# Performance work log

Measured on AMD Instinct MI355X. Metric: run time of the kernel, lower is better.

The kernel has to match this reference:

```python
import jax, jax.numpy as jnp
import numpy as np

B, L, C, K, NLEV, VOCAB, OUT = 32, 1024, 512, 2, 4, 128, 11


def setup_inputs() -> dict:
    key = jax.random.key(0)
    ks = jax.random.split(key, 8)
    x = jax.random.randint(ks[0], (B, L), 0, VOCAB, dtype=jnp.int32)
    mask = jax.random.randint(ks[1], (B, L), 0, 2).astype(jnp.bool_)
    emb = jax.random.uniform(ks[2], (VOCAB, C), minval=-0.5, maxval=0.5, dtype=jnp.float32)
    w1 = jax.random.normal(ks[3], (NLEV, C, C, K), dtype=jnp.float32) * 0.02
    b1 = jnp.zeros((NLEV, C), dtype=jnp.float32)
    w2 = jax.random.normal(ks[4], (NLEV, C, C, K), dtype=jnp.float32) * 0.02
    b2 = jnp.zeros((NLEV, C), dtype=jnp.float32)
    dec_w = jax.random.uniform(ks[5], (OUT, C), minval=-0.5, maxval=0.5, dtype=jnp.float32)
    dec_b = jnp.zeros((OUT,), dtype=jnp.float32)
    return dict(x=x, mask=mask, emb=emb, w1=w1, b1=b1, w2=w2, b2=b2, dec_w=dec_w, dec_b=dec_b)


def _causal_conv(h, w, b, dilation):
    # h: [B, C, L], w: [Cout, Cin, K]; left-pad (K-1)*d == conv+chomp in TCN
    pad = (w.shape[-1] - 1) * dilation
    out = jax.lax.conv_general_dilated(
        h, w, window_strides=(1,), padding=[(pad, 0)],
        rhs_dilation=(dilation,), dimension_numbers=("NCH", "OIH", "NCH"))
    return out + b[None, :, None]


def reference(x, mask, emb, w1, b1, w2, b2, dec_w, dec_b):
    h = emb[x].transpose(0, 2, 1)  # [B, C, L]
    for i in range(NLEV):  # fixed small number of TCN levels
        d = 2 ** i
        res = h
        h = jax.nn.relu(_causal_conv(h, w1[i], b1[i], d))
        h = jax.nn.relu(_causal_conv(h, w2[i], b2[i], d))
        h = jax.nn.relu(h + res)  # residual (in==out channels -> identity shortcut)
    y = jnp.einsum("bcl,oc->blo", h, dec_w) + dec_b  # [B, L, OUT]
    # mask-gather: original keeps only mask-true positions; zero others (jit-safe)
    return y * mask[..., None].astype(y.dtype)
```

## Files before the change

### kernel.cpp

```cpp
#include <hip/hip_runtime.h>
#include <stdint.h>

#define BB 32
#define LL 1024
#define CC 512
#define NN (BB * LL)
#define NLEVS 4
#define OUTD 11
#define LPAD 8
#define LROWS (LL + LPAD)

typedef __attribute__((ext_vector_type(8))) short bf16x8;
typedef __attribute__((ext_vector_type(4))) float f32x4;

static __device__ __forceinline__ unsigned short f2bf(float f) {
    union { float f; uint32_t u; } v; v.f = f;
    uint32_t u = v.u;
    uint32_t r = (u + 0x7fffu + ((u >> 16) & 1u)) >> 16;
    return (unsigned short)r;
}
static __device__ __forceinline__ float bf2f(unsigned short h) {
    union { uint32_t u; float f; } v; v.u = ((uint32_t)h) << 16;
    return v.f;
}

static __device__ __forceinline__ void llds16(const unsigned short* g, unsigned short* l) {
    __builtin_amdgcn_global_load_lds(
        (const __attribute__((address_space(1))) unsigned int*)g,
        (__attribute__((address_space(3))) unsigned int*)l, 16, 0, 0);
}

__global__ __launch_bounds__(256) void zero_pad_kernel(
    unsigned short* __restrict__ Hb0, unsigned short* __restrict__ Hb1)
{
    int t = blockIdx.x * 256 + threadIdx.x;
    unsigned short* base = (t >> 14) ? Hb1 : Hb0;
    int rem = t & 16383;
    int p = rem >> 9;
    int q = rem & 511;
    size_t off = (size_t)p * (LROWS * CC) + (size_t)q * 8;
    *(uint4*)(base + off) = (uint4){0u, 0u, 0u, 0u};
}

__global__ __launch_bounds__(256) void embed_kernel(
    const int* __restrict__ x, const float* __restrict__ emb,
    unsigned short* __restrict__ Hb0)
{
    int t = blockIdx.x * 256 + threadIdx.x;
    int n = t >> 6;
    int c8 = (t & 63) * 8;
    int idx = x[n];
    const float* src = emb + (size_t)idx * CC + c8;
    float4 v0 = *(const float4*)src;
    float4 v1 = *(const float4*)(src + 4);
    ushort4 a, b;
    a.x = f2bf(v0.x); a.y = f2bf(v0.y); a.z = f2bf(v0.z); a.w = f2bf(v0.w);
    b.x = f2bf(v1.x); b.y = f2bf(v1.y); b.z = f2bf(v1.z); b.w = f2bf(v1.w);
    int prow = (n >> 10) * LROWS + LPAD + (n & (LL - 1));
    unsigned short* dst = Hb0 + (size_t)prow * CC + c8;
    *(ushort4*)dst = a;
    *(ushort4*)(dst + 4) = b;
}

__global__ __launch_bounds__(256) void pack_w_kernel(
    const float* __restrict__ w1, const float* __restrict__ w2, unsigned short* __restrict__ WpT)
{
    int e = blockIdx.x * 256 + threadIdx.x;
    int cv = e >> 19;
    int r = e & 524287;
    int j = r >> 12;
    int co = (r >> 3) & 511;
    int h = r & 7;
    int kidx = j * 8 + h;
    int k = (kidx < 512) ? 1 : 0;
    int ci = kidx & 511;
    int lvl = cv >> 1;
    const float* w = (cv & 1) ? w2 : w1;
    float val = w[(((size_t)(lvl * 512 + co) * 512) + ci) * 2 + k];
    WpT[e] = f2bf(val);
}

template <bool HAS_RES>
__global__ __launch_bounds__(256, 4) void conv_gemm(
    const unsigned short* __restrict__ Ain, const unsigned short* __restrict__ WpT,
    const float* __restrict__ bias, const unsigned short* __restrict__ resB,
    unsigned short* __restrict__ OutB, int d)
{
    __shared__ unsigned short sA[136 * 64];

    const int tid = threadIdx.x;
    const int wave = tid >> 6, lane = tid & 63;

    const int bid = blockIdx.x;
    const int xcd = bid & 7;
    const int local = bid >> 3;
    const int cb = local >> 5;
    const int nb = xcd + 8 * (local & 31);
    const int co0 = cb * 128;
    const int n0 = nb * 128;

    const int rbase = (n0 >> 10) * LROWS + LPAD + (n0 & (LL - 1));
    const int r8 = lane >> 3;
    const int cswz = (lane & 7) ^ r8;
    const int wm = (wave >> 1) * 64;
    const int wn = (wave & 1) * 64;
    const int lm = lane & 15, quad = lane >> 4;

    f32x4 acc[4][4];
#pragma unroll
    for (int i = 0; i < 4; ++i)
#pragma unroll
        for (int j = 0; j < 4; ++j) acc[i][j] = (f32x4){0.f, 0.f, 0.f, 0.f};

    for (int it = 0; it < 8; ++it) {
        const int ci0 = it * 64;

        const unsigned short* gA = Ain + (size_t)(rbase - 8 + r8) * CC + ci0 + cswz * 8;
#pragma unroll
        for (int s4 = 0; s4 < 4; ++s4) {
            int s = s4 * 4 + wave;
            llds16(gA + (size_t)s * 8 * CC, sA + s * 8 * 64);
        }
        if (wave == 0) llds16(gA + (size_t)16 * 8 * CC, sA + 16 * 8 * 64);
        __syncthreads();

#pragma unroll
        for (int t = 0; t < 2; ++t) {
            const int shift = t ? d : 0;
            const int rowoff = 8 - shift + wm;
            const int key = (lm + 8 - shift) & 7;
#pragma unroll
            for (int kc = 0; kc < 2; ++kc) {
                const int jb = t * 64 + it * 8 + kc * 4 + quad;
                bf16x8 af[4], bfr[4];
#pragma unroll
                for (int mt = 0; mt < 4; ++mt) {
                    int row = rowoff + mt * 16 + lm;
                    af[mt] = *(const bf16x8*)&sA[row * 64 + (((kc * 4 + quad) ^ key) * 8)];
                }
                const unsigned short* bbase = WpT + ((size_t)jb * 512 + co0 + wn + lm) * 8;
#pragma unroll
                for (int nt = 0; nt < 4; ++nt)
                    bfr[nt] = *(const bf16x8*)(bbase + (size_t)nt * 16 * 8);
#pragma unroll
                for (int mt = 0; mt < 4; ++mt)
#pragma unroll
                    for (int nt = 0; nt < 4; ++nt)
                        acc[mt][nt] = __builtin_amdgcn_mfma_f32_16x16x32_bf16(
                            af[mt], bfr[nt], acc[mt][nt], 0, 0, 0);
            }
        }
        __syncthreads();
    }

    float bv[4];
#pragma unroll
    for (int nt = 0; nt < 4; ++nt) bv[nt] = bias[co0 + wn + nt * 16 + lm];

#pragma unroll
    for (int mt = 0; mt < 4; ++mt) {
        int prow0 = rbase + wm + mt * 16 + quad * 4;
#pragma unroll
        for (int nt = 0; nt < 4; ++nt) {
            int co = co0 + wn + nt * 16 + lm;
#pragma unroll
            for (int r = 0; r < 4; ++r) {
                size_t off = (size_t)(prow0 + r) * CC + co;
                float v = acc[mt][nt][r] + bv[nt];
                v = fmaxf(v, 0.f);
                if (HAS_RES) {
                    v += bf2f(resB[off]);
                    v = fmaxf(v, 0.f);
                }
                OutB[off] = f2bf(v);
            }
        }
    }
}

__global__ __launch_bounds__(256) void decode_kernel(
    const unsigned short* __restrict__ H, const float* __restrict__ dw,
    const float* __restrict__ db, const int* __restrict__ mask,
    float* __restrict__ out)
{
    __shared__ float sw[OUTD * CC];
    for (int i = threadIdx.x; i < OUTD * CC; i += 256) sw[i] = dw[i];
    __syncthreads();

    int wave = threadIdx.x >> 6, lane = threadIdx.x & 63;
    int n = blockIdx.x * 4 + wave;
    int prow = (n >> 10) * LROWS + LPAD + (n & (LL - 1));

    float hv[8];
#pragma unroll
    for (int j = 0; j < 8; ++j) hv[j] = bf2f(H[(size_t)prow * CC + lane + j * 64]);

    float accv[OUTD];
#pragma unroll
    for (int o = 0; o < OUTD; ++o) {
        float s = 0.f;
#pragma unroll
        for (int j = 0; j < 8; ++j) s += hv[j] * sw[o * CC + lane + j * 64];
        accv[o] = s;
    }
    float myv = 0.f;
#pragma unroll
    for (int o = 0; o < OUTD; ++o) {
        float s = accv[o];
#pragma unroll
        for (int m = 32; m; m >>= 1) s += __shfl_xor(s, m, 64);
        if (lane == o) myv = s;
    }
    if (lane < OUTD) {
        float mk = (mask[n] != 0) ? 1.f : 0.f;
        out[(size_t)n * OUTD + lane] = (myv + db[lane]) * mk;
    }
}

extern "C" void kernel_launch(void* const* d_in, const int* in_sizes, int n_in,
                              void* d_out, int out_size, void* d_ws, size_t ws_size,
                              hipStream_t stream)
{
    const int* x = (const int*)d_in[0];
    const int* mask = (const int*)d_in[1];
    const float* emb = (const float*)d_in[2];
    const float* w1 = (const float*)d_in[3];
    const float* b1 = (const float*)d_in[4];
    const float* w2 = (const float*)d_in[5];
    const float* b2 = (const float*)d_in[6];
    const float* dw = (const float*)d_in[7];
    const float* db = (const float*)d_in[8];
    float* out = (float*)d_out;

    char* ws = (char*)d_ws;
    const size_t HBB = (size_t)BB * LROWS * CC * 2;
    unsigned short* Hb0 = (unsigned short*)ws;
    unsigned short* Hb1 = (unsigned short*)(ws + HBB);
    unsigned short* WpT = (unsigned short*)(ws + 2 * HBB);

    zero_pad_kernel<<<128, 256, 0, stream>>>(Hb0, Hb1);
    embed_kernel<<<(NN * 64) / 256, 256, 0, stream>>>(x, emb, Hb0);
    pack_w_kernel<<<(NLEVS * 2 * CC * 1024) / 256, 256, 0, stream>>>(w1, w2, WpT);

    const int grid = (CC / 128) * (NN / 128);
    for (int i = 0; i < NLEVS; ++i) {
        int d = 1 << i;
        const unsigned short* W1 = WpT + (size_t)(i * 2 + 0) * CC * 1024;
        const unsigned short* W2 = WpT + (size_t)(i * 2 + 1) * CC * 1024;
        conv_gemm<false><<<grid, 256, 0, stream>>>(Hb0, W1, b1 + i * CC, nullptr, Hb1, d);
        conv_gemm<true><<<grid, 256, 0, stream>>>(Hb1, W2, b2 + i * CC, Hb0, Hb0, d);
    }
    decode_kernel<<<NN / 4, 256, 0, stream>>>(Hb0, dw, db, mask, out);
}
```

Measured before the change: 439.2 us.

## Switch conv GEMM to 32x32x16 MFMA with 128-wide K staging

Replaces the 16x16x32 bf16 MFMA tiling (4x4 tiles per wave) with 32x32x16 MFMA (2x2 tiles per wave). The K chunk staged in LDS doubles to 128 channels, so there are half as many barrier iterations, and the XOR swizzle is reworked for the wider rows. Per-wave fragment loads drop (2 A and 2 B per step instead of 4 each), which cuts LDS and global operand traffic per MFMA. The cost is double the LDS footprint, which may limit occupancy, and a new output-register mapping in the epilogue.

```diff
diff --git a/kernel.cpp b/kernel.cpp
--- a/kernel.cpp
+++ b/kernel.cpp
@@ -11,7 +11,7 @@
 #define LROWS (LL + LPAD)
 
 typedef __attribute__((ext_vector_type(8))) short bf16x8;
-typedef __attribute__((ext_vector_type(4))) float f32x4;
+typedef __attribute__((ext_vector_type(16))) float f32x16;
 
 static __device__ __forceinline__ unsigned short f2bf(float f) {
     union { float f; uint32_t u; } v; v.f = f;
@@ -86,7 +86,7 @@
     const float* __restrict__ bias, const unsigned short* __restrict__ resB,
     unsigned short* __restrict__ OutB, int d)
 {
-    __shared__ unsigned short sA[136 * 64];
+    __shared__ unsigned short sA[136 * 128];
 
     const int tid = threadIdx.x;
     const int wave = tid >> 6, lane = tid & 63;
@@ -100,73 +100,80 @@
     const int n0 = nb * 128;
 
     const int rbase = (n0 >> 10) * LROWS + LPAD + (n0 & (LL - 1));
-    const int r8 = lane >> 3;
-    const int cswz = (lane & 7) ^ r8;
     const int wm = (wave >> 1) * 64;
     const int wn = (wave & 1) * 64;
-    const int lm = lane & 15, quad = lane >> 4;
-
-    f32x4 acc[4][4];
-#pragma unroll
-    for (int i = 0; i < 4; ++i)
-#pragma unroll
-        for (int j = 0; j < 4; ++j) acc[i][j] = (f32x4){0.f, 0.f, 0.f, 0.f};
-
-    for (int it = 0; it < 8; ++it) {
-        const int ci0 = it * 64;
-
-        const unsigned short* gA = Ain + (size_t)(rbase - 8 + r8) * CC + ci0 + cswz * 8;
-#pragma unroll
-        for (int s4 = 0; s4 < 4; ++s4) {
-            int s = s4 * 4 + wave;
-            llds16(gA + (size_t)s * 8 * CC, sA + s * 8 * 64);
+    const int l31 = lane & 31;
+    const int g = lane >> 5;
+
+    const int r4 = lane >> 4;
+    const int c16 = lane & 15;
+
+    f32x16 acc[2][2];
+#pragma unroll
+    for (int i = 0; i < 2; ++i)
+#pragma unroll
+        for (int j = 0; j < 2; ++j)
+#pragma unroll
+            for (int e = 0; e < 16; ++e) acc[i][j][e] = 0.f;
+
+    for (int it = 0; it < 4; ++it) {
+        const int ci0 = it * 128;
+
+        for (int sg = wave; sg < 34; sg += 4) {
+            int rho = (4 * (sg & 1) + r4) & 7;
+            int cg = (c16 & 8) | ((c16 & 7) ^ rho);
+            const unsigned short* gA =
+                Ain + (size_t)(rbase - 8 + 4 * sg + r4) * CC + ci0 + cg * 8;
+            llds16(gA, sA + (4 * sg) * 128);
         }
-        if (wave == 0) llds16(gA + (size_t)16 * 8 * CC, sA + 16 * 8 * 64);
         __syncthreads();
 
 #pragma unroll
         for (int t = 0; t < 2; ++t) {
             const int shift = t ? d : 0;
             const int rowoff = 8 - shift + wm;
-            const int key = (lm + 8 - shift) & 7;
-#pragma unroll
-            for (int kc = 0; kc < 2; ++kc) {
-                const int jb = t * 64 + it * 8 + kc * 4 + quad;
-                bf16x8 af[4], bfr[4];
-#pragma unroll
-                for (int mt = 0; mt < 4; ++mt) {
-                    int row = rowoff + mt * 16 + lm;
-                    af[mt] = *(const bf16x8*)&sA[row * 64 + (((kc * 4 + quad) ^ key) * 8)];
+            const int key = ((lane & 7) + 8 - shift) & 7;
+#pragma unroll
+            for (int kk = 0; kk < 8; ++kk) {
+                const int c = 2 * kk + g;
+                const int cpos = (c & 8) | ((c & 7) ^ key);
+                const int jb = t * 64 + it * 16 + c;
+                bf16x8 af[2], bfr[2];
+#pragma unroll
+                for (int mt = 0; mt < 2; ++mt) {
+                    int row = rowoff + mt * 32 + l31;
+                    af[mt] = *(const bf16x8*)&sA[row * 128 + cpos * 8];
                 }
-                const unsigned short* bbase = WpT + ((size_t)jb * 512 + co0 + wn + lm) * 8;
-#pragma unroll
-                for (int nt = 0; nt < 4; ++nt)
-                    bfr[nt] = *(const bf16x8*)(bbase + (size_t)nt * 16 * 8);
-#pragma unroll
-                for (int mt = 0; mt < 4; ++mt)
-#pragma unroll
-                    for (int nt = 0; nt < 4; ++nt)
-                        acc[mt][nt] = __builtin_amdgcn_mfma_f32_16x16x32_bf16(
+                const unsigned short* bbase = WpT + ((size_t)jb * 512 + co0 + wn + l31) * 8;
+#pragma unroll
+                for (int nt = 0; nt < 2; ++nt)
+                    bfr[nt] = *(const bf16x8*)(bbase + (size_t)nt * 32 * 8);
+#pragma unroll
+                for (int mt = 0; mt < 2; ++mt)
+#pragma unroll
+                    for (int nt = 0; nt < 2; ++nt)
+                        acc[mt][nt] = __builtin_amdgcn_mfma_f32_32x32x16_bf16(
                             af[mt], bfr[nt], acc[mt][nt], 0, 0, 0);
             }
         }
         __syncthreads();
     }
 
-    float bv[4];
-#pragma unroll
-    for (int nt = 0; nt < 4; ++nt) bv[nt] = bias[co0 + wn + nt * 16 + lm];
-
-#pragma unroll
-    for (int mt = 0; mt < 4; ++mt) {
-        int prow0 = rbase + wm + mt * 16 + quad * 4;
-#pragma unroll
-        for (int nt = 0; nt < 4; ++nt) {
-            int co = co0 + wn + nt * 16 + lm;
-#pragma unroll
-            for (int r = 0; r < 4; ++r) {
-                size_t off = (size_t)(prow0 + r) * CC + co;
-                float v = acc[mt][nt][r] + bv[nt];
+    float bv[2];
+#pragma unroll
+    for (int nt = 0; nt < 2; ++nt) bv[nt] = bias[co0 + wn + nt * 32 + l31];
+
+#pragma unroll
+    for (int mt = 0; mt < 2; ++mt) {
+#pragma unroll
+        for (int nt = 0; nt < 2; ++nt) {
+            int co = co0 + wn + nt * 32 + l31;
+#pragma unroll
+            for (int reg = 0; reg < 16; ++reg) {
+                int rowIn = (reg & 3) + 8 * (reg >> 2) + 4 * g;
+                int prow = rbase + wm + mt * 32 + rowIn;
+                size_t off = (size_t)prow * CC + co;
+                float v = acc[mt][nt][reg] + bv[nt];
                 v = fmaxf(v, 0.f);
                 if (HAS_RES) {
                     v += bf2f(resB[off]);
```

New measurement: 446.4 us. Within noise of the previous version (+1.6%).

## Double K-chunk per LDS stage and software-prefetch A/B fragments in conv GEMM

Applied to the files above, without the earlier changes.

The conv GEMM now stages 128 input channels per LDS tile instead of 64, which halves the number of outer iterations and barrier pairs. The XOR swizzle is extended to 16-column groups to match the wider row. The inner loop becomes an 8-step software pipeline that loads the next A (LDS) and B (global) fragments while the MFMAs for the current step issue, hiding load latency. The costs are double the LDS, extra registers for the prefetch buffers, and an occupancy hint lowered from 4 to 3 blocks per SM.

```diff
diff --git a/kernel.cpp b/kernel.cpp
--- a/kernel.cpp
+++ b/kernel.cpp
@@ -81,12 +81,12 @@
 }
 
 template <bool HAS_RES>
-__global__ __launch_bounds__(256, 4) void conv_gemm(
+__global__ __launch_bounds__(256, 3) void conv_gemm(
     const unsigned short* __restrict__ Ain, const unsigned short* __restrict__ WpT,
     const float* __restrict__ bias, const unsigned short* __restrict__ resB,
     unsigned short* __restrict__ OutB, int d)
 {
-    __shared__ unsigned short sA[136 * 64];
+    __shared__ unsigned short sA[136 * 128];
 
     const int tid = threadIdx.x;
     const int wave = tid >> 6, lane = tid & 63;
@@ -100,54 +100,66 @@
     const int n0 = nb * 128;
 
     const int rbase = (n0 >> 10) * LROWS + LPAD + (n0 & (LL - 1));
-    const int r8 = lane >> 3;
-    const int cswz = (lane & 7) ^ r8;
     const int wm = (wave >> 1) * 64;
     const int wn = (wave & 1) * 64;
     const int lm = lane & 15, quad = lane >> 4;
 
+    const int r4 = lane >> 4;
+    const int c16 = lane & 15;
+
     f32x4 acc[4][4];
 #pragma unroll
     for (int i = 0; i < 4; ++i)
 #pragma unroll
         for (int j = 0; j < 4; ++j) acc[i][j] = (f32x4){0.f, 0.f, 0.f, 0.f};
 
-    for (int it = 0; it < 8; ++it) {
-        const int ci0 = it * 64;
-
-        const unsigned short* gA = Ain + (size_t)(rbase - 8 + r8) * CC + ci0 + cswz * 8;
-#pragma unroll
-        for (int s4 = 0; s4 < 4; ++s4) {
-            int s = s4 * 4 + wave;
-            llds16(gA + (size_t)s * 8 * CC, sA + s * 8 * 64);
+    for (int it = 0; it < 4; ++it) {
+        const int ci0 = it * 128;
+
+        for (int sg = wave; sg < 34; sg += 4) {
+            int rho = (4 * sg + r4) & 7;
+            int cg = (c16 & 8) | ((c16 & 7) ^ rho);
+            const unsigned short* gA =
+                Ain + (size_t)(rbase - 8 + 4 * sg + r4) * CC + ci0 + cg * 8;
+            llds16(gA, sA + (4 * sg) * 128);
         }
-        if (wave == 0) llds16(gA + (size_t)16 * 8 * CC, sA + 16 * 8 * 64);
         __syncthreads();
 
-#pragma unroll
-        for (int t = 0; t < 2; ++t) {
+        auto loadA = [&](int s, bf16x8* af) {
+            const int t = s >> 2, ks = s & 3;
             const int shift = t ? d : 0;
             const int rowoff = 8 - shift + wm;
-            const int key = (lm + 8 - shift) & 7;
-#pragma unroll
-            for (int kc = 0; kc < 2; ++kc) {
-                const int jb = t * 64 + it * 8 + kc * 4 + quad;
-                bf16x8 af[4], bfr[4];
-#pragma unroll
-                for (int mt = 0; mt < 4; ++mt) {
-                    int row = rowoff + mt * 16 + lm;
-                    af[mt] = *(const bf16x8*)&sA[row * 64 + (((kc * 4 + quad) ^ key) * 8)];
-                }
-                const unsigned short* bbase = WpT + ((size_t)jb * 512 + co0 + wn + lm) * 8;
+            const int key = (8 - shift + lm) & 7;
+            const int c = ks * 4 + quad;
+            const int cpos = (c & 8) | ((c & 7) ^ key);
+#pragma unroll
+            for (int mt = 0; mt < 4; ++mt)
+                af[mt] = *(const bf16x8*)&sA[(rowoff + mt * 16 + lm) * 128 + cpos * 8];
+        };
+        auto loadB = [&](int s, bf16x8* bf) {
+            const int t = s >> 2, ks = s & 3;
+            const int jb = t * 64 + it * 16 + ks * 4 + quad;
+            const unsigned short* bbase = WpT + ((size_t)jb * 512 + co0 + wn + lm) * 8;
+#pragma unroll
+            for (int nt = 0; nt < 4; ++nt)
+                bf[nt] = *(const bf16x8*)(bbase + (size_t)nt * 16 * 8);
+        };
+
+        bf16x8 afc[4], bfc[4], afn[4], bfn[4];
+        loadA(0, afc);
+        loadB(0, bfc);
+#pragma unroll
+        for (int s = 0; s < 8; ++s) {
+            if (s < 7) { loadA(s + 1, afn); loadB(s + 1, bfn); }
+#pragma unroll
+            for (int mt = 0; mt < 4; ++mt)
 #pragma unroll
                 for (int nt = 0; nt < 4; ++nt)
-                    bfr[nt] = *(const bf16x8*)(bbase + (size_t)nt * 16 * 8);
-#pragma unroll
-                for (int mt = 0; mt < 4; ++mt)
-#pragma unroll
-                    for (int nt = 0; nt < 4; ++nt)
-                        acc[mt][nt] = __builtin_amdgcn_mfma_f32_16x16x32_bf16(
-                            af[mt], bfr[nt], acc[mt][nt], 0, 0, 0);
+                    acc[mt][nt] = __builtin_amdgcn_mfma_f32_16x16x32_bf16(
+                        afc[mt], bfc[nt], acc[mt][nt], 0, 0, 0);
+            if (s < 7) {
+#pragma unroll
+                for (int q2 = 0; q2 < 4; ++q2) { afc[q2] = afn[q2]; bfc[q2] = bfn[q2]; }
             }
         }
         __syncthreads();
```

New measurement: 419.7 us. 1.05x faster.
